# Optimization experiments

Measured on AMD Instinct MI355X. Metric: run time of the kernel, lower is better.

## Reference

```python
import jax, jax.numpy as jnp
import numpy as np

B, L, D, H = 4, 1024, 768, 12
HD = D // H  # head_dim = 64
SCALING = HD ** -0.5


def setup_inputs() -> dict:
    key = jax.random.key(0)
    ks = jax.random.split(key, 6)
    x = jax.random.normal(ks[0], (B, L, D), dtype=jnp.float32)
    attn_bias = jax.random.normal(ks[1], (B, H, L, L), dtype=jnp.float32)
    s_in = 1.0 / np.sqrt(D)
    w_in = jax.random.uniform(ks[2], (3 * D, D), dtype=jnp.float32, minval=-s_in, maxval=s_in)
    b_in = jax.random.uniform(ks[3], (3 * D,), dtype=jnp.float32, minval=-s_in, maxval=s_in)
    w_out = jax.random.uniform(ks[4], (D, D), dtype=jnp.float32, minval=-s_in, maxval=s_in)
    b_out = jax.random.uniform(ks[5], (D,), dtype=jnp.float32, minval=-s_in, maxval=s_in)
    return {"x": x, "attn_bias": attn_bias, "w_in": w_in, "b_in": b_in,
            "w_out": w_out, "b_out": b_out}


def reference(x, attn_bias, w_in, b_in, w_out, b_out):
    # fused QKV projection: [B, L, 3D]
    qkv = jnp.einsum('bld,ed->ble', x, w_in) + b_in
    q, k, v = jnp.split(qkv, 3, axis=-1)
    # [B, H, L, HD]
    q = q.reshape(B, L, H, HD).transpose(0, 2, 1, 3) * SCALING
    k = k.reshape(B, L, H, HD).transpose(0, 2, 1, 3)
    v = v.reshape(B, L, H, HD).transpose(0, 2, 1, 3)
    # bias-augmented attention scores: [B, H, L, L]
    scores = jnp.einsum('bhqd,bhkd->bhqk', q, k) + attn_bias
    probs = jax.nn.softmax(scores, axis=-1)
    # attend: [B, H, L, HD] -> [B, L, D]
    o = jnp.einsum('bhqk,bhkd->bhqd', probs, v)
    o = o.transpose(0, 2, 1, 3).reshape(B, L, D)
    return jnp.einsum('bld,ed->ble', o, w_out) + b_out
```

## Files before the change

### kernel.cpp

```cpp
#include <hip/hip_runtime.h>
#include <hip/hip_bf16.h>
#include <stdint.h>

#define B_ 4
#define L_ 1024
#define D_ 768
#define H_ 12
#define HD_ 64
#define M_ 4096
#define N3_ 2304

typedef float f32x4 __attribute__((ext_vector_type(4)));
typedef float f32x4v __attribute__((ext_vector_type(4)));
typedef short bf16x8 __attribute__((ext_vector_type(8)));
typedef unsigned short u16;
typedef u16 u16x8 __attribute__((ext_vector_type(8)));
typedef u16 u16x4 __attribute__((ext_vector_type(4)));
typedef uint32_t u32x2 __attribute__((ext_vector_type(2)));

#define AS3 __attribute__((address_space(3)))
#define AS1 __attribute__((address_space(1)))

__device__ __forceinline__ void gll16(const void* g, void* l) {
  __builtin_amdgcn_global_load_lds((const AS1 void*)g, (AS3 void*)l, 16, 0, 0);
}

__device__ __forceinline__ u16 f2bf(float f) {
  uint32_t u = __builtin_bit_cast(uint32_t, f);
  u += 0x7fffu + ((u >> 16) & 1u);
  return (u16)(u >> 16);
}

__global__ void k_cvt3(const float* __restrict__ a, u16* __restrict__ ao, int na4,
                       const float* __restrict__ b, u16* __restrict__ bo, int nb4,
                       const float* __restrict__ c, u16* __restrict__ co, int nc4) {
  int i = blockIdx.x * 256 + threadIdx.x;
  const float* src;
  u16* dst;
  if (i < na4) {
    src = a; dst = ao;
  } else if (i < na4 + nb4) {
    src = b; dst = bo; i -= na4;
  } else if (i < na4 + nb4 + nc4) {
    src = c; dst = co; i -= na4 + nb4;
  } else {
    return;
  }
  f32x4v v = ((const f32x4v*)src)[i];
  u16x4 o;
  o.x = f2bf(v.x); o.y = f2bf(v.y); o.z = f2bf(v.z); o.w = f2bf(v.w);
  ((u16x4*)dst)[i] = o;
}

__global__ __launch_bounds__(256) void k_gemm_qkv(
    const u16* __restrict__ Xb, const u16* __restrict__ Wb,
    const float* __restrict__ b_in,
    u16* __restrict__ gQ, u16* __restrict__ gK, u16* __restrict__ gV) {
  __shared__ u16 As[128 * 64];
  __shared__ u16 Bs[128 * 64];
  const int tid = threadIdx.x;
  const int lane = tid & 63;
  const int w = tid >> 6;
  const int wm = (w >> 1) * 64;
  const int wn = (w & 1) * 64;
  const int lr = lane & 15;
  const int lg = lane >> 4;
  const int m0 = blockIdx.x * 128;
  const int n0 = blockIdx.y * 128;

  f32x4 acc[4][4];
#pragma unroll
  for (int i = 0; i < 4; ++i)
#pragma unroll
    for (int j = 0; j < 4; ++j) acc[i][j] = (f32x4){0.f, 0.f, 0.f, 0.f};

  for (int kt = 0; kt < 12; ++kt) {
    __syncthreads();
#pragma unroll
    for (int i = 0; i < 4; ++i) {
      int seg = i * 256 + tid;
      int row = seg >> 3;
      int sl = (seg & 7) ^ (row & 7);
      gll16(Xb + (size_t)(m0 + row) * 768 + kt * 64 + sl * 8, (char*)As + seg * 16);
      gll16(Wb + (size_t)(n0 + row) * 768 + kt * 64 + sl * 8, (char*)Bs + seg * 16);
    }
    __syncthreads();
#pragma unroll
    for (int kh = 0; kh < 2; ++kh) {
      bf16x8 af[4], bfr[4];
#pragma unroll
      for (int t = 0; t < 4; ++t) {
        int ra = wm + t * 16 + lr;
        af[t] = *(const bf16x8*)((const char*)As + ra * 128 +
                                 ((kh * 64 + lg * 16) ^ ((ra & 7) << 4)));
        int rb = wn + t * 16 + lr;
        bfr[t] = *(const bf16x8*)((const char*)Bs + rb * 128 +
                                  ((kh * 64 + lg * 16) ^ ((rb & 7) << 4)));
      }
#pragma unroll
      for (int mi = 0; mi < 4; ++mi)
#pragma unroll
        for (int ni = 0; ni < 4; ++ni)
          acc[mi][ni] = __builtin_amdgcn_mfma_f32_16x16x32_bf16(
              af[mi], bfr[ni], acc[mi][ni], 0, 0, 0);
    }
  }
  const int sec = blockIdx.y / 6;
  u16* dst = sec == 0 ? gQ : (sec == 1 ? gK : gV);
  const float scale = sec == 0 ? 0.125f : 1.0f;
#pragma unroll
  for (int ni = 0; ni < 4; ++ni) {
    int e = n0 + wn + ni * 16 + lr;
    float bias = b_in[e];
    int es = e - sec * 768;
    int h = es >> 6, d = es & 63;
#pragma unroll
    for (int mi = 0; mi < 4; ++mi) {
#pragma unroll
      for (int j = 0; j < 4; ++j) {
        int m = m0 + wm + mi * 16 + lg * 4 + j;
        int bb = m >> 10, lq = m & 1023;
        float vv = (acc[mi][ni][j] + bias) * scale;
        dst[(size_t)((bb * 12 + h) * 1024 + lq) * 64 + d] = f2bf(vv);
      }
    }
  }
}

__global__ __launch_bounds__(256) void k_transpose(const u16* __restrict__ V,
                                                   u16* __restrict__ Vt) {
  __shared__ u16 t[64][66];
  const int tid = threadIdx.x;
  const int bh = blockIdx.x >> 4;
  const int kv0 = (blockIdx.x & 15) * 64;
  {
    int r = tid >> 2, c0 = (tid & 3) * 16;
    const u16* src = V + (size_t)(bh * 1024 + kv0 + r) * 64 + c0;
#pragma unroll
    for (int p = 0; p < 2; ++p) {
      u16x8 x = *(const u16x8*)(src + p * 8);
#pragma unroll
      for (int e = 0; e < 8; ++e) t[r][c0 + p * 8 + e] = x[e];
    }
  }
  __syncthreads();
  {
    int d = tid >> 2, k0 = (tid & 3) * 16;
    u16* dst = Vt + (size_t)(bh * 64 + d) * 1024 + kv0 + k0;
#pragma unroll
    for (int p = 0; p < 2; ++p) {
      u16x8 o;
#pragma unroll
      for (int e = 0; e < 8; ++e) o[e] = t[k0 + p * 8 + e][d];
      *(u16x8*)(dst + p * 8) = o;
    }
  }
}

__global__ __launch_bounds__(256) void k_attn(
    const u16* __restrict__ gQ, const u16* __restrict__ gK,
    const u16* __restrict__ gVt, const float* __restrict__ gBias,
    u16* __restrict__ gO) {
  __shared__ u16 Ks[2][64 * 64];
  __shared__ u16 Vs[2][64 * 64];
  __shared__ float Bi[2][64 * 64];
  __shared__ f32x4 PlV[4][128];
  const int tid = threadIdx.x;
  const int lane = tid & 63;
  const int w = tid >> 6;
  const int lr = lane & 15;
  const int lg = lane >> 4;
  const int lb = (blockIdx.x & 7) * 96 + (blockIdx.x >> 3);
  const int bh = lb >> 4;
  const int q0 = (lb & 15) * 64;
  const int qr = q0 + w * 16;

#define STAGE(buf, kv0)                                                        \
  do {                                                                         \
    _Pragma("unroll") for (int i_ = 0; i_ < 2; ++i_) {                         \
      int seg_ = i_ * 256 + tid;                                               \
      int row_ = seg_ >> 3;                                                    \
      int sl_ = (seg_ & 7) ^ (row_ & 7);                                       \
      gll16(gK + (size_t)(bh * 1024 + (kv0) + row_) * 64 + sl_ * 8,            \
            (char*)Ks[buf] + seg_ * 16);                                       \
      gll16(gVt + (size_t)(bh * 64 + row_) * 1024 + (kv0) + sl_ * 8,           \
            (char*)Vs[buf] + seg_ * 16);                                       \
    }                                                                          \
    _Pragma("unroll") for (int i_ = 0; i_ < 4; ++i_) {                         \
      int seg_ = i_ * 256 + tid;                                               \
      int qrow_ = seg_ >> 4;                                                   \
      int c_ = (seg_ & 15) ^ (qrow_ & 7);                                      \
      gll16(gBias + (size_t)(bh * 1024 + q0 + qrow_) * 1024 + (kv0) + c_ * 4,  \
            (char*)Bi[buf] + seg_ * 16);                                       \
    }                                                                          \
  } while (0)

  bf16x8 qa[2];
#pragma unroll
  for (int kh = 0; kh < 2; ++kh)
    qa[kh] = *(const bf16x8*)(gQ + (size_t)(bh * 1024 + qr + lr) * 64 + kh * 32 + lg * 8);

  f32x4 oacc[4];
#pragma unroll
  for (int dt = 0; dt < 4; ++dt) oacc[dt] = (f32x4){0.f, 0.f, 0.f, 0.f};
  float mrow = -1e30f, lrow = 0.f;

  char* plw = (char*)PlV[w];
  const int swz = (lr & 7) << 4;

  STAGE(0, 0);
  __syncthreads();

  for (int t = 0; t < 16; ++t) {
    const int cur = t & 1;
    if (t < 15) STAGE(cur ^ 1, (t + 1) * 64);

    f32x4 s[4];
#pragma unroll
    for (int ni = 0; ni < 4; ++ni) s[ni] = (f32x4){0.f, 0.f, 0.f, 0.f};
    __builtin_amdgcn_s_setprio(1);
#pragma unroll
    for (int kh = 0; kh < 2; ++kh)
#pragma unroll
      for (int ni = 0; ni < 4; ++ni) {
        int rk = ni * 16 + lr;
        bf16x8 kb = *(const bf16x8*)((const char*)Ks[cur] + rk * 128 +
                                     ((kh * 64 + lg * 16) ^ ((rk & 7) << 4)));
        s[ni] = __builtin_amdgcn_mfma_f32_16x16x32_bf16(kb, qa[kh], s[ni], 0, 0, 0);
      }
    __builtin_amdgcn_s_setprio(0);

#pragma unroll
    for (int ni = 0; ni < 4; ++ni) {
      f32x4 bv = *(const f32x4*)((const char*)Bi[cur] + (w * 16 + lr) * 256 +
                                 (((ni * 4 + lg) ^ (lr & 7)) << 4));
      s[ni] += bv;
    }

    float mx0 = fmaxf(fmaxf(s[0][0], s[0][1]), fmaxf(s[0][2], s[0][3]));
    float mx1 = fmaxf(fmaxf(s[1][0], s[1][1]), fmaxf(s[1][2], s[1][3]));
    float mx2 = fmaxf(fmaxf(s[2][0], s[2][1]), fmaxf(s[2][2], s[2][3]));
    float mx3 = fmaxf(fmaxf(s[3][0], s[3][1]), fmaxf(s[3][2], s[3][3]));
    float vmax = fmaxf(fmaxf(mx0, mx1), fmaxf(mx2, mx3));
    vmax = fmaxf(vmax, __shfl_xor(vmax, 16));
    vmax = fmaxf(vmax, __shfl_xor(vmax, 32));
    float mnew = fmaxf(mrow, vmax);
    float al = __expf(mrow - mnew);
    mrow = mnew;
#pragma unroll
    for (int ni = 0; ni < 4; ++ni)
#pragma unroll
      for (int j = 0; j < 4; ++j) s[ni][j] = __expf(s[ni][j] - mnew);
    float r0 = (s[0][0] + s[0][1]) + (s[0][2] + s[0][3]);
    float r1 = (s[1][0] + s[1][1]) + (s[1][2] + s[1][3]);
    float r2 = (s[2][0] + s[2][1]) + (s[2][2] + s[2][3]);
    float r3 = (s[3][0] + s[3][1]) + (s[3][2] + s[3][3]);
    float rs = (r0 + r1) + (r2 + r3);
    rs += __shfl_xor(rs, 16);
    rs += __shfl_xor(rs, 32);
    lrow = lrow * al + rs;

    f32x4 av;
#pragma unroll
    for (int j = 0; j < 4; ++j) av[j] = __shfl(al, (lane & 48) | (lg * 4 + j));
#pragma unroll
    for (int dt = 0; dt < 4; ++dt) oacc[dt] *= av;

#pragma unroll
    for (int ni = 0; ni < 4; ++ni) {
      uint32_t w0 = (uint32_t)f2bf(s[ni][0]) | ((uint32_t)f2bf(s[ni][1]) << 16);
      uint32_t w1 = (uint32_t)f2bf(s[ni][2]) | ((uint32_t)f2bf(s[ni][3]) << 16);
      u32x2 pv = {w0, w1};
      *(u32x2*)(plw + lr * 128 + ((ni * 32 + lg * 8) ^ swz)) = pv;
    }
    __builtin_amdgcn_s_setprio(1);
#pragma unroll
    for (int kh = 0; kh < 2; ++kh) {
      bf16x8 pa = *(const bf16x8*)(plw + lr * 128 + ((kh * 64 + lg * 16) ^ swz));
#pragma unroll
      for (int dt = 0; dt < 4; ++dt) {
        int rv = dt * 16 + lr;
        bf16x8 vb = *(const bf16x8*)((const char*)Vs[cur] + rv * 128 +
                                     ((kh * 64 + lg * 16) ^ ((rv & 7) << 4)));
        oacc[dt] = __builtin_amdgcn_mfma_f32_16x16x32_bf16(pa, vb, oacc[dt], 0, 0, 0);
      }
    }
    __builtin_amdgcn_s_setprio(0);

    __syncthreads();
  }

  float inv = 1.0f / lrow;
  f32x4 iv;
#pragma unroll
  for (int j = 0; j < 4; ++j) iv[j] = __shfl(inv, (lane & 48) | (lg * 4 + j));
  const int bg = bh / 12, h = bh % 12;
#pragma unroll
  for (int j = 0; j < 4; ++j) {
    int row = qr + lg * 4 + j;
#pragma unroll
    for (int dt = 0; dt < 4; ++dt) {
      gO[(size_t)(bg * 1024 + row) * 768 + h * 64 + dt * 16 + lr] =
          f2bf(oacc[dt][j] * iv[j]);
    }
  }
#undef STAGE
}

__global__ __launch_bounds__(256) void k_gemm_out(
    const u16* __restrict__ Ob, const u16* __restrict__ Wb,
    const float* __restrict__ b_out, float* __restrict__ out) {
  __shared__ u16 As[64 * 64];
  __shared__ u16 Bs[64 * 64];
  const int tid = threadIdx.x;
  const int lane = tid & 63;
  const int w = tid >> 6;
  const int wm = (w >> 1) * 32;
  const int wn = (w & 1) * 32;
  const int lr = lane & 15;
  const int lg = lane >> 4;
  const int m0 = blockIdx.x * 64;
  const int n0 = blockIdx.y * 64;

  f32x4 acc[2][2];
#pragma unroll
  for (int i = 0; i < 2; ++i)
#pragma unroll
    for (int j = 0; j < 2; ++j) acc[i][j] = (f32x4){0.f, 0.f, 0.f, 0.f};

  for (int kt = 0; kt < 12; ++kt) {
    __syncthreads();
#pragma unroll
    for (int i = 0; i < 2; ++i) {
      int seg = i * 256 + tid;
      int row = seg >> 3;
      int sl = (seg & 7) ^ (row & 7);
      gll16(Ob + (size_t)(m0 + row) * 768 + kt * 64 + sl * 8, (char*)As + seg * 16);
      gll16(Wb + (size_t)(n0 + row) * 768 + kt * 64 + sl * 8, (char*)Bs + seg * 16);
    }
    __syncthreads();
#pragma unroll
    for (int kh = 0; kh < 2; ++kh) {
      bf16x8 af[2], bfr[2];
#pragma unroll
      for (int t = 0; t < 2; ++t) {
        int ra = wm + t * 16 + lr;
        af[t] = *(const bf16x8*)((const char*)As + ra * 128 +
                                 ((kh * 64 + lg * 16) ^ ((ra & 7) << 4)));
        int rb = wn + t * 16 + lr;
        bfr[t] = *(const bf16x8*)((const char*)Bs + rb * 128 +
                                  ((kh * 64 + lg * 16) ^ ((rb & 7) << 4)));
      }
#pragma unroll
      for (int mi = 0; mi < 2; ++mi)
#pragma unroll
        for (int ni = 0; ni < 2; ++ni)
          acc[mi][ni] = __builtin_amdgcn_mfma_f32_16x16x32_bf16(
              af[mi], bfr[ni], acc[mi][ni], 0, 0, 0);
    }
  }
#pragma unroll
  for (int ni = 0; ni < 2; ++ni) {
    int n = n0 + wn + ni * 16 + lr;
    float bias = b_out[n];
#pragma unroll
    for (int mi = 0; mi < 2; ++mi) {
#pragma unroll
      for (int j = 0; j < 4; ++j) {
        int m = m0 + wm + mi * 16 + lg * 4 + j;
        out[(size_t)m * 768 + n] = acc[mi][ni][j] + bias;
      }
    }
  }
}

extern "C" void kernel_launch(void* const* d_in, const int* in_sizes, int n_in,
                              void* d_out, int out_size, void* d_ws, size_t ws_size,
                              hipStream_t stream) {
  const float* x = (const float*)d_in[0];
  const float* attn_bias = (const float*)d_in[1];
  const float* w_in = (const float*)d_in[2];
  const float* b_in = (const float*)d_in[3];
  const float* w_out = (const float*)d_in[4];
  const float* b_out = (const float*)d_in[5];
  float* out = (float*)d_out;

  char* ws = (char*)d_ws;
  size_t off = 0;
  u16* xb = (u16*)(ws + off);  off += (size_t)M_ * D_ * 2;
  u16* wib = (u16*)(ws + off); off += (size_t)N3_ * D_ * 2;
  u16* wob = (u16*)(ws + off); off += (size_t)D_ * D_ * 2;
  u16* q = (u16*)(ws + off);   off += (size_t)48 * 1024 * 64 * 2;
  u16* k = (u16*)(ws + off);   off += (size_t)48 * 1024 * 64 * 2;
  u16* v = (u16*)(ws + off);   off += (size_t)48 * 1024 * 64 * 2;
  u16* vt = (u16*)(ws + off);  off += (size_t)48 * 1024 * 64 * 2;
  u16* ob = (u16*)(ws + off);  off += (size_t)M_ * D_ * 2;

  const int na4 = (M_ * D_) / 4;
  const int nb4 = (N3_ * D_) / 4;
  const int nc4 = (D_ * D_) / 4;
  k_cvt3<<<(na4 + nb4 + nc4 + 255) / 256, 256, 0, stream>>>(
      x, xb, na4, w_in, wib, nb4, w_out, wob, nc4);
  k_gemm_qkv<<<dim3(32, 18), 256, 0, stream>>>(xb, wib, b_in, q, k, v);
  k_transpose<<<768, 256, 0, stream>>>(v, vt);
  k_attn<<<768, 256, 0, stream>>>(q, k, vt, attn_bias, ob);
  k_gemm_out<<<dim3(64, 12), 256, 0, stream>>>(ob, wob, b_out, out);
}
```

Baseline: 121.8 us.

## Triple-buffer attention bias prefetch and replace full syncs with partial vmcnt waits

The attention kernel now splits staging into K/V loads (double-buffered) and bias loads (triple-buffered, prefetched two tiles ahead). The P scratch tile reuses the current bias buffer region instead of a separate LDS array. Each iteration ends with a barrier preceded by `s_waitcnt vmcnt(4)` rather than `__syncthreads`, so the newest bias prefetch can stay in flight across the barrier. This targets latency on the large fp32 bias stream. In exchange, LDS per block grows and correctness depends on hand-counted vmcnt values.

```diff
diff --git a/kernel.cpp b/kernel.cpp
--- a/kernel.cpp
+++ b/kernel.cpp
@@ -163,8 +163,7 @@
     u16* __restrict__ gO) {
   __shared__ u16 Ks[2][64 * 64];
   __shared__ u16 Vs[2][64 * 64];
-  __shared__ float Bi[2][64 * 64];
-  __shared__ f32x4 PlV[4][128];
+  __shared__ float Bi[3][64 * 64];
   const int tid = threadIdx.x;
   const int lane = tid & 63;
   const int w = tid >> 6;
@@ -175,7 +174,7 @@
   const int q0 = (lb & 15) * 64;
   const int qr = q0 + w * 16;
 
-#define STAGE(buf, kv0)                                                        \
+#define STAGE_KV(buf, kv0)                                                     \
   do {                                                                         \
     _Pragma("unroll") for (int i_ = 0; i_ < 2; ++i_) {                         \
       int seg_ = i_ * 256 + tid;                                               \
@@ -186,6 +185,10 @@
       gll16(gVt + (size_t)(bh * 64 + row_) * 1024 + (kv0) + sl_ * 8,           \
             (char*)Vs[buf] + seg_ * 16);                                       \
     }                                                                          \
+  } while (0)
+
+#define STAGE_BI(buf, kv0)                                                     \
+  do {                                                                         \
     _Pragma("unroll") for (int i_ = 0; i_ < 4; ++i_) {                         \
       int seg_ = i_ * 256 + tid;                                               \
       int qrow_ = seg_ >> 4;                                                   \
@@ -205,15 +208,19 @@
   for (int dt = 0; dt < 4; ++dt) oacc[dt] = (f32x4){0.f, 0.f, 0.f, 0.f};
   float mrow = -1e30f, lrow = 0.f;
 
-  char* plw = (char*)PlV[w];
   const int swz = (lr & 7) << 4;
 
-  STAGE(0, 0);
-  __syncthreads();
+  STAGE_KV(0, 0);
+  STAGE_BI(0, 0);
+  STAGE_BI(1, 64);
+  asm volatile("s_waitcnt vmcnt(4)" ::: "memory");
+  __builtin_amdgcn_s_barrier();
 
   for (int t = 0; t < 16; ++t) {
-    const int cur = t & 1;
-    if (t < 15) STAGE(cur ^ 1, (t + 1) * 64);
+    const int cur2 = t & 1;
+    const int cur3 = t % 3;
+    if (t < 15) STAGE_KV(cur2 ^ 1, (t + 1) * 64);
+    if (t < 14) STAGE_BI((t + 2) % 3, (t + 2) * 64);
 
     f32x4 s[4];
 #pragma unroll
@@ -224,7 +231,7 @@
 #pragma unroll
       for (int ni = 0; ni < 4; ++ni) {
         int rk = ni * 16 + lr;
-        bf16x8 kb = *(const bf16x8*)((const char*)Ks[cur] + rk * 128 +
+        bf16x8 kb = *(const bf16x8*)((const char*)Ks[cur2] + rk * 128 +
                                      ((kh * 64 + lg * 16) ^ ((rk & 7) << 4)));
         s[ni] = __builtin_amdgcn_mfma_f32_16x16x32_bf16(kb, qa[kh], s[ni], 0, 0, 0);
       }
@@ -232,7 +239,7 @@
 
 #pragma unroll
     for (int ni = 0; ni < 4; ++ni) {
-      f32x4 bv = *(const f32x4*)((const char*)Bi[cur] + (w * 16 + lr) * 256 +
+      f32x4 bv = *(const f32x4*)((const char*)Bi[cur3] + (w * 16 + lr) * 256 +
                                  (((ni * 4 + lg) ^ (lr & 7)) << 4));
       s[ni] += bv;
     }
@@ -266,6 +273,7 @@
 #pragma unroll
     for (int dt = 0; dt < 4; ++dt) oacc[dt] *= av;
 
+    char* plw = (char*)Bi[cur3] + w * 4096;
 #pragma unroll
     for (int ni = 0; ni < 4; ++ni) {
       uint32_t w0 = (uint32_t)f2bf(s[ni][0]) | ((uint32_t)f2bf(s[ni][1]) << 16);
@@ -280,14 +288,20 @@
 #pragma unroll
       for (int dt = 0; dt < 4; ++dt) {
         int rv = dt * 16 + lr;
-        bf16x8 vb = *(const bf16x8*)((const char*)Vs[cur] + rv * 128 +
+        bf16x8 vb = *(const bf16x8*)((const char*)Vs[cur2] + rv * 128 +
                                      ((kh * 64 + lg * 16) ^ ((rv & 7) << 4)));
         oacc[dt] = __builtin_amdgcn_mfma_f32_16x16x32_bf16(pa, vb, oacc[dt], 0, 0, 0);
       }
     }
     __builtin_amdgcn_s_setprio(0);
 
-    __syncthreads();
+    if (t <= 13) {
+      asm volatile("s_waitcnt vmcnt(4)" ::: "memory");
+      __builtin_amdgcn_s_barrier();
+    } else if (t == 14) {
+      asm volatile("s_waitcnt vmcnt(0)" ::: "memory");
+      __builtin_amdgcn_s_barrier();
+    }
   }
 
   float inv = 1.0f / lrow;
@@ -304,7 +318,8 @@
           f2bf(oacc[dt][j] * iv[j]);
     }
   }
-#undef STAGE
+#undef STAGE_KV
+#undef STAGE_BI
 }
 
 __global__ __launch_bounds__(256) void k_gemm_out(
```

After: 123.8 us. About the same (+1.6%).

## Process 128 query rows per attention block and load bias directly into registers

Applied to the files above, without the earlier changes.

The attention kernel now handles 128 query rows per block: each wave computes two 16-row tiles that share the same K/V shared-memory tiles, which halves the K/V staging traffic and halves the grid to 384 blocks. The bias is no longer staged through shared memory with async copies. Each lane loads its bias fragment straight from global memory into registers, prefetched one tile ahead. This frees the large bias LDS buffer but raises register pressure, and leaves fewer blocks to fill the GPU's compute units.

```diff
diff --git a/kernel.cpp b/kernel.cpp
--- a/kernel.cpp
+++ b/kernel.cpp
@@ -163,19 +163,19 @@
     u16* __restrict__ gO) {
   __shared__ u16 Ks[2][64 * 64];
   __shared__ u16 Vs[2][64 * 64];
-  __shared__ float Bi[2][64 * 64];
-  __shared__ f32x4 PlV[4][128];
+  __shared__ f32x4 PlV[4][256];
   const int tid = threadIdx.x;
   const int lane = tid & 63;
   const int w = tid >> 6;
   const int lr = lane & 15;
   const int lg = lane >> 4;
-  const int lb = (blockIdx.x & 7) * 96 + (blockIdx.x >> 3);
-  const int bh = lb >> 4;
-  const int q0 = (lb & 15) * 64;
-  const int qr = q0 + w * 16;
-
-#define STAGE(buf, kv0)                                                        \
+  const int lb = (blockIdx.x & 7) * 48 + (blockIdx.x >> 3);
+  const int bh = lb >> 3;
+  const int q0 = (lb & 7) * 128;
+  const int qr0 = q0 + w * 16;
+  const int qr1 = q0 + 64 + w * 16;
+
+#define STAGE_KV(buf, kv0)                                                     \
   do {                                                                         \
     _Pragma("unroll") for (int i_ = 0; i_ < 2; ++i_) {                         \
       int seg_ = i_ * 256 + tid;                                               \
@@ -186,38 +186,47 @@
       gll16(gVt + (size_t)(bh * 64 + row_) * 1024 + (kv0) + sl_ * 8,           \
             (char*)Vs[buf] + seg_ * 16);                                       \
     }                                                                          \
-    _Pragma("unroll") for (int i_ = 0; i_ < 4; ++i_) {                         \
-      int seg_ = i_ * 256 + tid;                                               \
-      int qrow_ = seg_ >> 4;                                                   \
-      int c_ = (seg_ & 15) ^ (qrow_ & 7);                                      \
-      gll16(gBias + (size_t)(bh * 1024 + q0 + qrow_) * 1024 + (kv0) + c_ * 4,  \
-            (char*)Bi[buf] + seg_ * 16);                                       \
-    }                                                                          \
   } while (0)
 
-  bf16x8 qa[2];
-#pragma unroll
-  for (int kh = 0; kh < 2; ++kh)
-    qa[kh] = *(const bf16x8*)(gQ + (size_t)(bh * 1024 + qr + lr) * 64 + kh * 32 + lg * 8);
-
-  f32x4 oacc[4];
-#pragma unroll
-  for (int dt = 0; dt < 4; ++dt) oacc[dt] = (f32x4){0.f, 0.f, 0.f, 0.f};
-  float mrow = -1e30f, lrow = 0.f;
+  const float* bline0 = gBias + (size_t)(bh * 1024 + qr0 + lr) * 1024;
+  const float* bline1 = gBias + (size_t)(bh * 1024 + qr1 + lr) * 1024;
+
+  bf16x8 qa[2][2];
+#pragma unroll
+  for (int kh = 0; kh < 2; ++kh) {
+    qa[0][kh] = *(const bf16x8*)(gQ + (size_t)(bh * 1024 + qr0 + lr) * 64 + kh * 32 + lg * 8);
+    qa[1][kh] = *(const bf16x8*)(gQ + (size_t)(bh * 1024 + qr1 + lr) * 64 + kh * 32 + lg * 8);
+  }
+
+  f32x4 oacc[2][4];
+#pragma unroll
+  for (int p = 0; p < 2; ++p)
+#pragma unroll
+    for (int dt = 0; dt < 4; ++dt) oacc[p][dt] = (f32x4){0.f, 0.f, 0.f, 0.f};
+  float mrow[2] = {-1e30f, -1e30f}, lrow[2] = {0.f, 0.f};
 
   char* plw = (char*)PlV[w];
   const int swz = (lr & 7) << 4;
 
-  STAGE(0, 0);
+  STAGE_KV(0, 0);
+  f32x4 bcur[2][4];
+#pragma unroll
+  for (int ni = 0; ni < 4; ++ni) {
+    bcur[0][ni] = *(const f32x4*)(bline0 + ni * 16 + lg * 4);
+    bcur[1][ni] = *(const f32x4*)(bline1 + ni * 16 + lg * 4);
+  }
   __syncthreads();
 
   for (int t = 0; t < 16; ++t) {
     const int cur = t & 1;
-    if (t < 15) STAGE(cur ^ 1, (t + 1) * 64);
-
-    f32x4 s[4];
-#pragma unroll
-    for (int ni = 0; ni < 4; ++ni) s[ni] = (f32x4){0.f, 0.f, 0.f, 0.f};
+    const int kv0 = t * 64;
+    if (t < 15) STAGE_KV(cur ^ 1, kv0 + 64);
+
+    f32x4 s[2][4];
+#pragma unroll
+    for (int p = 0; p < 2; ++p)
+#pragma unroll
+      for (int ni = 0; ni < 4; ++ni) s[p][ni] = (f32x4){0.f, 0.f, 0.f, 0.f};
     __builtin_amdgcn_s_setprio(1);
 #pragma unroll
     for (int kh = 0; kh < 2; ++kh)
@@ -226,63 +235,78 @@
         int rk = ni * 16 + lr;
         bf16x8 kb = *(const bf16x8*)((const char*)Ks[cur] + rk * 128 +
                                      ((kh * 64 + lg * 16) ^ ((rk & 7) << 4)));
-        s[ni] = __builtin_amdgcn_mfma_f32_16x16x32_bf16(kb, qa[kh], s[ni], 0, 0, 0);
+        s[0][ni] = __builtin_amdgcn_mfma_f32_16x16x32_bf16(kb, qa[0][kh], s[0][ni], 0, 0, 0);
+        s[1][ni] = __builtin_amdgcn_mfma_f32_16x16x32_bf16(kb, qa[1][kh], s[1][ni], 0, 0, 0);
       }
     __builtin_amdgcn_s_setprio(0);
 
 #pragma unroll
     for (int ni = 0; ni < 4; ++ni) {
-      f32x4 bv = *(const f32x4*)((const char*)Bi[cur] + (w * 16 + lr) * 256 +
-                                 (((ni * 4 + lg) ^ (lr & 7)) << 4));
-      s[ni] += bv;
-    }
-
-    float mx0 = fmaxf(fmaxf(s[0][0], s[0][1]), fmaxf(s[0][2], s[0][3]));
-    float mx1 = fmaxf(fmaxf(s[1][0], s[1][1]), fmaxf(s[1][2], s[1][3]));
-    float mx2 = fmaxf(fmaxf(s[2][0], s[2][1]), fmaxf(s[2][2], s[2][3]));
-    float mx3 = fmaxf(fmaxf(s[3][0], s[3][1]), fmaxf(s[3][2], s[3][3]));
-    float vmax = fmaxf(fmaxf(mx0, mx1), fmaxf(mx2, mx3));
-    vmax = fmaxf(vmax, __shfl_xor(vmax, 16));
-    vmax = fmaxf(vmax, __shfl_xor(vmax, 32));
-    float mnew = fmaxf(mrow, vmax);
-    float al = __expf(mrow - mnew);
-    mrow = mnew;
-#pragma unroll
-    for (int ni = 0; ni < 4; ++ni)
-#pragma unroll
-      for (int j = 0; j < 4; ++j) s[ni][j] = __expf(s[ni][j] - mnew);
-    float r0 = (s[0][0] + s[0][1]) + (s[0][2] + s[0][3]);
-    float r1 = (s[1][0] + s[1][1]) + (s[1][2] + s[1][3]);
-    float r2 = (s[2][0] + s[2][1]) + (s[2][2] + s[2][3]);
-    float r3 = (s[3][0] + s[3][1]) + (s[3][2] + s[3][3]);
-    float rs = (r0 + r1) + (r2 + r3);
-    rs += __shfl_xor(rs, 16);
-    rs += __shfl_xor(rs, 32);
-    lrow = lrow * al + rs;
-
-    f32x4 av;
-#pragma unroll
-    for (int j = 0; j < 4; ++j) av[j] = __shfl(al, (lane & 48) | (lg * 4 + j));
-#pragma unroll
-    for (int dt = 0; dt < 4; ++dt) oacc[dt] *= av;
-
-#pragma unroll
-    for (int ni = 0; ni < 4; ++ni) {
-      uint32_t w0 = (uint32_t)f2bf(s[ni][0]) | ((uint32_t)f2bf(s[ni][1]) << 16);
-      uint32_t w1 = (uint32_t)f2bf(s[ni][2]) | ((uint32_t)f2bf(s[ni][3]) << 16);
-      u32x2 pv = {w0, w1};
-      *(u32x2*)(plw + lr * 128 + ((ni * 32 + lg * 8) ^ swz)) = pv;
+      s[0][ni] += bcur[0][ni];
+      s[1][ni] += bcur[1][ni];
+    }
+    if (t < 15) {
+#pragma unroll
+      for (int ni = 0; ni < 4; ++ni) {
+        bcur[0][ni] = *(const f32x4*)(bline0 + kv0 + 64 + ni * 16 + lg * 4);
+        bcur[1][ni] = *(const f32x4*)(bline1 + kv0 + 64 + ni * 16 + lg * 4);
+      }
+    }
+
+#pragma unroll
+    for (int p = 0; p < 2; ++p) {
+      float mx0 = fmaxf(fmaxf(s[p][0][0], s[p][0][1]), fmaxf(s[p][0][2], s[p][0][3]));
+      float mx1 = fmaxf(fmaxf(s[p][1][0], s[p][1][1]), fmaxf(s[p][1][2], s[p][1][3]));
+      float mx2 = fmaxf(fmaxf(s[p][2][0], s[p][2][1]), fmaxf(s[p][2][2], s[p][2][3]));
+      float mx3 = fmaxf(fmaxf(s[p][3][0], s[p][3][1]), fmaxf(s[p][3][2], s[p][3][3]));
+      float vmax = fmaxf(fmaxf(mx0, mx1), fmaxf(mx2, mx3));
+      vmax = fmaxf(vmax, __shfl_xor(vmax, 16));
+      vmax = fmaxf(vmax, __shfl_xor(vmax, 32));
+      float mnew = fmaxf(mrow[p], vmax);
+      float al = __expf(mrow[p] - mnew);
+      mrow[p] = mnew;
+#pragma unroll
+      for (int ni = 0; ni < 4; ++ni)
+#pragma unroll
+        for (int j = 0; j < 4; ++j) s[p][ni][j] = __expf(s[p][ni][j] - mnew);
+      float r0 = (s[p][0][0] + s[p][0][1]) + (s[p][0][2] + s[p][0][3]);
+      float r1 = (s[p][1][0] + s[p][1][1]) + (s[p][1][2] + s[p][1][3]);
+      float r2 = (s[p][2][0] + s[p][2][1]) + (s[p][2][2] + s[p][2][3]);
+      float r3 = (s[p][3][0] + s[p][3][1]) + (s[p][3][2] + s[p][3][3]);
+      float rs = (r0 + r1) + (r2 + r3);
+      rs += __shfl_xor(rs, 16);
+      rs += __shfl_xor(rs, 32);
+      lrow[p] = lrow[p] * al + rs;
+      f32x4 av;
+#pragma unroll
+      for (int j = 0; j < 4; ++j) av[j] = __shfl(al, (lane & 48) | (lg * 4 + j));
+#pragma unroll
+      for (int dt = 0; dt < 4; ++dt) oacc[p][dt] *= av;
+    }
+
+#pragma unroll
+    for (int p = 0; p < 2; ++p) {
+      char* pl = plw + p * 2048;
+#pragma unroll
+      for (int ni = 0; ni < 4; ++ni) {
+        uint32_t w0 = (uint32_t)f2bf(s[p][ni][0]) | ((uint32_t)f2bf(s[p][ni][1]) << 16);
+        uint32_t w1 = (uint32_t)f2bf(s[p][ni][2]) | ((uint32_t)f2bf(s[p][ni][3]) << 16);
+        u32x2 pv = {w0, w1};
+        *(u32x2*)(pl + lr * 128 + ((ni * 32 + lg * 8) ^ swz)) = pv;
+      }
     }
     __builtin_amdgcn_s_setprio(1);
 #pragma unroll
     for (int kh = 0; kh < 2; ++kh) {
-      bf16x8 pa = *(const bf16x8*)(plw + lr * 128 + ((kh * 64 + lg * 16) ^ swz));
+      bf16x8 pa0 = *(const bf16x8*)(plw + lr * 128 + ((kh * 64 + lg * 16) ^ swz));
+      bf16x8 pa1 = *(const bf16x8*)(plw + 2048 + lr * 128 + ((kh * 64 + lg * 16) ^ swz));
 #pragma unroll
       for (int dt = 0; dt < 4; ++dt) {
         int rv = dt * 16 + lr;
         bf16x8 vb = *(const bf16x8*)((const char*)Vs[cur] + rv * 128 +
                                      ((kh * 64 + lg * 16) ^ ((rv & 7) << 4)));
-        oacc[dt] = __builtin_amdgcn_mfma_f32_16x16x32_bf16(pa, vb, oacc[dt], 0, 0, 0);
+        oacc[0][dt] = __builtin_amdgcn_mfma_f32_16x16x32_bf16(pa0, vb, oacc[0][dt], 0, 0, 0);
+        oacc[1][dt] = __builtin_amdgcn_mfma_f32_16x16x32_bf16(pa1, vb, oacc[1][dt], 0, 0, 0);
       }
     }
     __builtin_amdgcn_s_setprio(0);
@@ -290,21 +314,25 @@
     __syncthreads();
   }
 
-  float inv = 1.0f / lrow;
-  f32x4 iv;
-#pragma unroll
-  for (int j = 0; j < 4; ++j) iv[j] = __shfl(inv, (lane & 48) | (lg * 4 + j));
   const int bg = bh / 12, h = bh % 12;
 #pragma unroll
-  for (int j = 0; j < 4; ++j) {
-    int row = qr + lg * 4 + j;
-#pragma unroll
-    for (int dt = 0; dt < 4; ++dt) {
-      gO[(size_t)(bg * 1024 + row) * 768 + h * 64 + dt * 16 + lr] =
-          f2bf(oacc[dt][j] * iv[j]);
-    }
-  }
-#undef STAGE
+  for (int p = 0; p < 2; ++p) {
+    float inv = 1.0f / lrow[p];
+    f32x4 iv;
+#pragma unroll
+    for (int j = 0; j < 4; ++j) iv[j] = __shfl(inv, (lane & 48) | (lg * 4 + j));
+    const int qrp = p == 0 ? qr0 : qr1;
+#pragma unroll
+    for (int j = 0; j < 4; ++j) {
+      int row = qrp + lg * 4 + j;
+#pragma unroll
+      for (int dt = 0; dt < 4; ++dt) {
+        gO[(size_t)(bg * 1024 + row) * 768 + h * 64 + dt * 16 + lr] =
+            f2bf(oacc[p][dt][j] * iv[j]);
+      }
+    }
+  }
+#undef STAGE_KV
 }
 
 __global__ __launch_bounds__(256) void k_gemm_out(
@@ -403,6 +431,6 @@
       x, xb, na4, w_in, wib, nb4, w_out, wob, nc4);
   k_gemm_qkv<<<dim3(32, 18), 256, 0, stream>>>(xb, wib, b_in, q, k, v);
   k_transpose<<<768, 256, 0, stream>>>(v, vt);
-  k_attn<<<768, 256, 0, stream>>>(q, k, vt, attn_bias, ob);
+  k_attn<<<384, 256, 0, stream>>>(q, k, vt, attn_bias, ob);
   k_gemm_out<<<dim3(64, 12), 256, 0, stream>>>(ob, wob, b_out, out);
 }
```

Result: faster. 115.8 us (-5.0%).
